# Kernel optimization log

Measured on AMD Instinct MI355X. Metric: run time of the kernel, lower is better.

The kernel has to match this reference:

```python
import jax, jax.numpy as jnp
import numpy as np

BN_EPS = 1e-5


def _gcn_layer(x, adj_norm, W, b, gamma, beta):
    # x: [B,T,V,C], adj_norm: [B,V,V] (identical per time step, as in the torch expand)
    x = jnp.einsum('bvw,btwc->btvc', adj_norm, x)
    x = jnp.einsum('btvc,co->btvo', x, W) + b
    # BatchNorm1d in training mode: biased batch stats over (B, T*V) per channel
    mean = x.mean(axis=(0, 1, 2))
    var = x.var(axis=(0, 1, 2))
    x = (x - mean) * jax.lax.rsqrt(var + BN_EPS) * gamma + beta
    return jax.nn.relu(x)


def _forward(x, adjacency, w1, b1, g1, be1, w2, b2, g2, be2, tw, tb, f1w, f1b, f2w, f2b):
    # degree-normalized adjacency: D^-1/2 A D^-1/2 (computed once; the torch
    # code recomputes the identical result inside B*T python loops)
    deg = adjacency.sum(axis=-1, keepdims=True)                # [B,V,1]
    dis = jnp.power(deg + 1e-6, -0.5)
    adj_norm = dis * adjacency * jnp.swapaxes(dis, -1, -2)     # [B,V,V]
    x1 = _gcn_layer(x, adj_norm, w1, b1, g1, be1)
    x2 = _gcn_layer(x1, adj_norm, w2, b2, g2, be2)
    x = x1 + x2                                                # [B,T,V,H]
    B, T, V, C = x.shape
    x = x.transpose(0, 2, 3, 1).reshape(B, V * C, T)           # [B, V*H, T]
    x = jax.lax.conv_general_dilated(
        x, tw, window_strides=(1,), padding=[(1, 1)],
        dimension_numbers=('NCH', 'OIH', 'NCH')) + tb[None, :, None]
    x = x.mean(axis=-1)                                        # [B, tcn_hidden]
    # dropout is identity in eval mode
    x = jax.nn.relu(x @ f1w + f1b)
    return x @ f2w + f2b


def setup_inputs() -> dict:
    key = jax.random.key(0)
    ks = jax.random.split(key, 12)
    B, T, V, Cin, H, TC, NC, K = 16, 512, 64, 16, 64, 256, 10, 3
    s = 0.05
    return {
        'x': jax.random.normal(ks[0], (B, T, V, Cin), jnp.float32),
        'adjacency': jax.random.uniform(ks[1], (B, V, V), jnp.float32),
        'w1': jax.random.normal(ks[2], (Cin, H), jnp.float32) * s,
        'b1': jnp.zeros((H,), jnp.float32),
        'g1': jnp.ones((H,), jnp.float32),
        'be1': jnp.zeros((H,), jnp.float32),
        'w2': jax.random.normal(ks[3], (H, H), jnp.float32) * s,
        'b2': jnp.zeros((H,), jnp.float32),
        'g2': jnp.ones((H,), jnp.float32),
        'be2': jnp.zeros((H,), jnp.float32),
        'tw': jax.random.normal(ks[4], (TC, H * V, K), jnp.float32) * 0.01,
        'tb': jnp.zeros((TC,), jnp.float32),
        'f1w': jax.random.normal(ks[5], (TC, TC // 2), jnp.float32) * s,
        'f1b': jnp.zeros((TC // 2,), jnp.float32),
        'f2w': jax.random.normal(ks[6], (TC // 2, NC), jnp.float32) * s,
        'f2b': jnp.zeros((NC,), jnp.float32),
    }


def reference(x, adjacency, w1, b1, g1, be1, w2, b2, g2, be2, tw, tb, f1w, f1b, f2w, f2b):
    return _forward(x, adjacency, w1, b1, g1, be1, w2, b2, g2, be2, tw, tb, f1w, f1b, f2w, f2b)
```

## Files before the change

kernel.cpp:

```cpp
#include <hip/hip_runtime.h>

#define B_   16
#define T_   512
#define V_   64
#define C1_  16
#define H_   64
#define TC_  256
#define NC_  10
#define INV_N (1.0f/524288.0f)
#define INV_T (1.0f/512.0f)

__global__ __launch_bounds__(256) void k_adjnorm(const float* __restrict__ adj,
                                                 float* __restrict__ AnT,
                                                 float* __restrict__ statsP) {
  const int b = blockIdx.x;
  __shared__ float As[4096];
  __shared__ float dis[64];
  for (int idx = threadIdx.x; idx < 4096; idx += 256) As[idx] = adj[b * 4096 + idx];
  __syncthreads();
  if (threadIdx.x < 64) {
    const int v = threadIdx.x;
    float s = 0.f;
    #pragma unroll 8
    for (int w = 0; w < 64; ++w) s += As[v * 64 + ((w + v) & 63)];
    dis[v] = rsqrtf(s + 1e-6f);
  }
  __syncthreads();
  for (int idx = threadIdx.x; idx < 4096; idx += 256) {
    const int v = idx >> 6, w = idx & 63;
    AnT[b * 4096 + w * 64 + v] = dis[v] * As[v * 64 + w] * dis[w];
  }
  if (threadIdx.x < 128) statsP[b * 128 + threadIdx.x] = 0.f;
}

__global__ __launch_bounds__(256) void k_gcn1(const float* __restrict__ x,
    const float* __restrict__ AnT, float* __restrict__ y) {
  const int b    = blockIdx.y;
  const int lane = threadIdx.x & 63;
  const int wq   = __builtin_amdgcn_readfirstlane(threadIdx.x >> 6);
  const float* __restrict__ At = AnT + b * 4096;
  for (int k = 0; k < 2; ++k) {
    const int t = blockIdx.x * 8 + wq * 2 + k;
    const float* __restrict__ xt = x + ((size_t)(b * T_ + t)) * V_ * C1_;
    float Y[16];
    #pragma unroll
    for (int i = 0; i < 16; ++i) Y[i] = 0.f;
    for (int w = 0; w < V_; ++w) {
      const float a = At[w * 64 + lane];
      const float* __restrict__ xr = xt + w * C1_;
      #pragma unroll
      for (int c = 0; c < 16; ++c) Y[c] += a * xr[c];
    }
    float4* yo = (float4*)(y + (((size_t)(b * T_ + t)) * V_ + lane) * C1_);
    yo[0] = make_float4(Y[0], Y[1], Y[2], Y[3]);
    yo[1] = make_float4(Y[4], Y[5], Y[6], Y[7]);
    yo[2] = make_float4(Y[8], Y[9], Y[10], Y[11]);
    yo[3] = make_float4(Y[12], Y[13], Y[14], Y[15]);
  }
}

__global__ __launch_bounds__(256) void k_stats1(const float* __restrict__ y,
    const float* __restrict__ w1, const float* __restrict__ b1,
    float* __restrict__ statsP) {
  const int lane = threadIdx.x & 63;
  const int wq   = __builtin_amdgcn_readfirstlane(threadIdx.x >> 6);
  float w1col[16];
  #pragma unroll
  for (int c = 0; c < 16; ++c) w1col[c] = w1[c * 64 + lane];
  const float bb = b1[lane];
  float ts0 = 0.f, ts1 = 0.f;
  const int row0 = blockIdx.x * 512 + wq * 128;
  for (int r = 0; r < 128; ++r) {
    const float* __restrict__ yr = y + (size_t)(row0 + r) * C1_;
    float z = bb;
    #pragma unroll
    for (int c = 0; c < 16; ++c) z += yr[c] * w1col[c];
    ts0 += z; ts1 += z * z;
  }
  __shared__ float sred[4][128];
  sred[wq][lane]      = ts0;
  sred[wq][64 + lane] = ts1;
  __syncthreads();
  if (threadIdx.x < 128) {
    const float v = sred[0][threadIdx.x] + sred[1][threadIdx.x] +
                    sred[2][threadIdx.x] + sred[3][threadIdx.x];
    atomicAdd(&statsP[(blockIdx.x & 7) * 128 + threadIdx.x], v);
  }
}

__global__ __launch_bounds__(256, 3) void k_gcn2(const float* __restrict__ y,
    const float* __restrict__ AnT, const float* __restrict__ w1,
    const float* __restrict__ b1, const float* __restrict__ g1,
    const float* __restrict__ be1, const float* __restrict__ w2,
    const float* __restrict__ b2, float* __restrict__ statsP,
    float* __restrict__ z2) {
  __shared__ float x1s[4096];
  __shared__ float Pt[64][65];
  __shared__ float aff[128];
  const int b    = blockIdx.y;
  const int t0   = blockIdx.x * 4;
  const int lane = threadIdx.x & 63;
  const int wq   = __builtin_amdgcn_readfirstlane(threadIdx.x >> 6);
  const int q0   = wq * 16;
  if (threadIdx.x < 64) {
    const int c = threadIdx.x;
    float s0 = 0.f, s1 = 0.f;
    #pragma unroll
    for (int s = 0; s < 8; ++s) { s0 += statsP[s * 128 + c]; s1 += statsP[s * 128 + 64 + c]; }
    const float mean = s0 * INV_N;
    const float var  = s1 * INV_N - mean * mean;
    const float sc   = g1[c] * rsqrtf(var + 1e-5f);
    aff[c]      = sc;
    aff[64 + c] = be1[c] - mean * sc + sc * b1[c];
  }
  __syncthreads();
  const float sc1 = aff[lane];
  const float shb = aff[64 + lane];
  float w1col[16];
  #pragma unroll
  for (int c = 0; c < 16; ++c) w1col[c] = w1[c * 64 + lane];
  const float* __restrict__ At = AnT + b * 4096;
  float ts0[16], ts1[16];
  #pragma unroll
  for (int i = 0; i < 16; ++i) { ts0[i] = 0.f; ts1[i] = 0.f; }

  for (int tt = 0; tt < 4; ++tt) {
    const int t = t0 + tt;
    const float* __restrict__ yt = y + ((size_t)(b * T_ + t)) * V_ * C1_;
    #pragma unroll
    for (int k = 0; k < 16; ++k) {
      const int w = q0 + k;
      const float* __restrict__ yr = yt + w * C1_;
      float z = 0.f;
      #pragma unroll
      for (int c = 0; c < 16; ++c) z += yr[c] * w1col[c];
      x1s[w * 64 + lane] = fmaxf(z * sc1 + shb, 0.f);
    }
    __syncthreads();
    float P[16];
    #pragma unroll
    for (int i = 0; i < 16; ++i) P[i] = 0.f;
    for (int w = 0; w < 64; ++w) {
      const float xv = x1s[w * 64 + lane];
      const float* __restrict__ ar = At + w * 64 + q0;
      #pragma unroll
      for (int i = 0; i < 16; ++i) P[i] += ar[i] * xv;
    }
    #pragma unroll
    for (int i = 0; i < 16; ++i) Pt[lane][q0 + i] = P[i];
    __syncthreads();
    float Z[16];
    #pragma unroll
    for (int i = 0; i < 16; ++i) Z[i] = b2[q0 + i];
    for (int c = 0; c < 64; ++c) {
      const float p = Pt[c][lane];
      const float* __restrict__ wr = w2 + c * 64 + q0;
      #pragma unroll
      for (int i = 0; i < 16; ++i) Z[i] += p * wr[i];
    }
    #pragma unroll
    for (int i = 0; i < 16; ++i) { const float v = Z[i]; ts0[i] += v; ts1[i] += v * v; }
    float4* zo = (float4*)(z2 + (((size_t)(b * T_ + t)) * V_ + lane) * H_ + q0);
    zo[0] = make_float4(Z[0], Z[1], Z[2], Z[3]);
    zo[1] = make_float4(Z[4], Z[5], Z[6], Z[7]);
    zo[2] = make_float4(Z[8], Z[9], Z[10], Z[11]);
    zo[3] = make_float4(Z[12], Z[13], Z[14], Z[15]);
    __syncthreads();
  }
  #pragma unroll
  for (int i = 0; i < 16; ++i) {
    float s0 = ts0[i], s1 = ts1[i];
    for (int off = 32; off > 0; off >>= 1) {
      s0 += __shfl_down(s0, off, 64);
      s1 += __shfl_down(s1, off, 64);
    }
    if (lane == 0) {
      atomicAdd(&statsP[(8 + (blockIdx.x & 7)) * 128 + q0 + i], s0);
      atomicAdd(&statsP[(8 + (blockIdx.x & 7)) * 128 + 64 + q0 + i], s1);
    }
  }
}

__global__ __launch_bounds__(256) void k_sfl(const float* __restrict__ y,
    const float* __restrict__ z2, const float* __restrict__ statsP,
    const float* __restrict__ w1, const float* __restrict__ b1,
    const float* __restrict__ g1, const float* __restrict__ be1,
    const float* __restrict__ g2, const float* __restrict__ be2,
    float* __restrict__ S, float* __restrict__ F, float* __restrict__ L) {
  const int b = blockIdx.y, v = blockIdx.x;
  const int c  = threadIdx.x & 63;
  const int wq = __builtin_amdgcn_readfirstlane(threadIdx.x >> 6);
  float s0 = 0.f, s1 = 0.f, u0 = 0.f, u1 = 0.f;
  #pragma unroll
  for (int s = 0; s < 8; ++s) {
    s0 += statsP[s * 128 + c];       s1 += statsP[s * 128 + 64 + c];
    u0 += statsP[(8 + s) * 128 + c]; u1 += statsP[(8 + s) * 128 + 64 + c];
  }
  const float m1 = s0 * INV_N, va1 = s1 * INV_N - m1 * m1;
  const float sc1  = g1[c] * rsqrtf(va1 + 1e-5f);
  const float shb1 = be1[c] - m1 * sc1 + sc1 * b1[c];
  const float m2 = u0 * INV_N, va2 = u1 * INV_N - m2 * m2;
  const float sc2 = g2[c] * rsqrtf(va2 + 1e-5f);
  const float sh2 = be2[c] - m2 * sc2;
  float w1col[16];
  #pragma unroll
  for (int cc = 0; cc < 16; ++cc) w1col[cc] = w1[cc * 64 + c];

  float acc = 0.f, fv = 0.f, lv = 0.f;
  for (int t = wq; t < T_; t += 4) {
    const size_t row = ((size_t)(b * T_ + t)) * V_ + v;
    const float* __restrict__ yr = y + row * C1_;
    float z1v = 0.f;
    #pragma unroll
    for (int cc = 0; cc < 16; ++cc) z1v += yr[cc] * w1col[cc];
    const float x1 = fmaxf(z1v * sc1 + shb1, 0.f);
    const float x2 = fmaxf(z2[row * H_ + c] * sc2 + sh2, 0.f);
    const float xs = x1 + x2;
    acc += xs;
    if (t == 0) fv = xs;
    if (t == T_ - 1) lv = xs;
  }
  __shared__ float red[4][64];
  red[wq][c] = acc;
  __syncthreads();
  const int o = (b * V_ + v) * 64 + c;
  if (wq == 0) { S[o] = red[0][c] + red[1][c] + red[2][c] + red[3][c]; F[o] = fv; }
  if (wq == 3) L[o] = lv;
}

__global__ __launch_bounds__(256) void k_pool(const float* __restrict__ S,
    const float* __restrict__ F, const float* __restrict__ L,
    const float* __restrict__ twt, float* __restrict__ mp) {
  const int cog = blockIdx.x;
  const int kc  = blockIdx.y;
  const int ci0 = kc * 256;
  __shared__ float a_s[3][16 * 260];
  for (int f4 = threadIdx.x; f4 < 3072; f4 += 256) {
    const int arr = f4 >> 10;
    const int rem = f4 & 1023;
    const int bb  = rem >> 6;
    const int ci4 = rem & 63;
    const float4 sv = *(const float4*)&S[bb * 4096 + ci0 + ci4 * 4];
    float4 o;
    if (arr == 0) {
      const float4 lv = *(const float4*)&L[bb * 4096 + ci0 + ci4 * 4];
      o = make_float4(sv.x - lv.x, sv.y - lv.y, sv.z - lv.z, sv.w - lv.w);
    } else if (arr == 1) {
      o = sv;
    } else {
      const float4 fvv = *(const float4*)&F[bb * 4096 + ci0 + ci4 * 4];
      o = make_float4(sv.x - fvv.x, sv.y - fvv.y, sv.z - fvv.z, sv.w - fvv.w);
    }
    *(float4*)&a_s[arr][bb * 260 + ci4 * 4] = o;
  }
  __syncthreads();
  const int bb   = threadIdx.x & 15;
  const int co   = threadIdx.x >> 4;
  const int co_g = cog * 16 + co;
  float acc = 0.f;
  for (int ci4 = 0; ci4 < 64; ++ci4) {
    const float4 a0 = *(const float4*)&a_s[0][bb * 260 + ci4 * 4];
    const float4 a1 = *(const float4*)&a_s[1][bb * 260 + ci4 * 4];
    const float4 a2 = *(const float4*)&a_s[2][bb * 260 + ci4 * 4];
    const float4* tp = (const float4*)(twt + ((size_t)co_g * 4096 + ci0 + ci4 * 4) * 3);
    const float4 f0 = tp[0], f1 = tp[1], f2 = tp[2];
    acc += f0.x * a0.x + f0.y * a1.x + f0.z * a2.x
         + f0.w * a0.y + f1.x * a1.y + f1.y * a2.y
         + f1.z * a0.z + f1.w * a1.z + f2.x * a2.z
         + f2.y * a0.w + f2.z * a1.w + f2.w * a2.w;
  }
  mp[kc * 4096 + bb * 256 + co_g] = acc;
}

__global__ __launch_bounds__(128) void k_head(const float* __restrict__ mp,
    const float* __restrict__ tb, const float* __restrict__ f1w,
    const float* __restrict__ f1b, const float* __restrict__ f2w,
    const float* __restrict__ f2b, float* __restrict__ out) {
  const int b = blockIdx.x;
  __shared__ float ms[256];
  __shared__ float hs[128];
  for (int co = threadIdx.x; co < 256; co += 128) {
    float s = 0.f;
    #pragma unroll
    for (int kc = 0; kc < 16; ++kc) s += mp[kc * 4096 + b * 256 + co];
    ms[co] = s * INV_T + tb[co];
  }
  __syncthreads();
  {
    const int j = threadIdx.x;
    float acc = f1b[j];
    #pragma unroll 8
    for (int k = 0; k < 256; ++k) acc += ms[k] * f1w[k * 128 + j];
    hs[j] = fmaxf(acc, 0.f);
  }
  __syncthreads();
  if (threadIdx.x < NC_) {
    const int n = threadIdx.x;
    float acc = f2b[n];
    #pragma unroll 8
    for (int j = 0; j < 128; ++j) acc += hs[j] * f2w[j * NC_ + n];
    out[b * NC_ + n] = acc;
  }
}

extern "C" void kernel_launch(void* const* d_in, const int* in_sizes, int n_in,
                              void* d_out, int out_size, void* d_ws, size_t ws_size,
                              hipStream_t stream) {
  const float* x   = (const float*)d_in[0];
  const float* adj = (const float*)d_in[1];
  const float* w1  = (const float*)d_in[2];
  const float* b1  = (const float*)d_in[3];
  const float* g1  = (const float*)d_in[4];
  const float* be1 = (const float*)d_in[5];
  const float* w2  = (const float*)d_in[6];
  const float* b2  = (const float*)d_in[7];
  const float* g2  = (const float*)d_in[8];
  const float* be2 = (const float*)d_in[9];
  const float* twt = (const float*)d_in[10];
  const float* tb  = (const float*)d_in[11];
  const float* f1w = (const float*)d_in[12];
  const float* f1b = (const float*)d_in[13];
  const float* f2w = (const float*)d_in[14];
  const float* f2b = (const float*)d_in[15];
  float* out = (float*)d_out;
  float* ws  = (float*)d_ws;

  float* AnT    = ws;
  float* statsP = ws + 65536;
  float* S      = ws + 67584;
  float* F      = ws + 133120;
  float* L      = ws + 198656;
  float* mp     = ws + 264192;
  float* y      = ws + 329728;
  float* z2     = y + (size_t)B_ * T_ * V_ * C1_;

  hipLaunchKernelGGL(k_adjnorm, dim3(B_), dim3(256), 0, stream, adj, AnT, statsP);
  hipLaunchKernelGGL(k_gcn1, dim3(T_ / 8, B_), dim3(256), 0, stream, x, AnT, y);
  hipLaunchKernelGGL(k_stats1, dim3(1024), dim3(256), 0, stream, y, w1, b1, statsP);
  hipLaunchKernelGGL(k_gcn2, dim3(T_ / 4, B_), dim3(256), 0, stream,
                     y, AnT, w1, b1, g1, be1, w2, b2, statsP, z2);
  hipLaunchKernelGGL(k_sfl, dim3(V_, B_), dim3(256), 0, stream,
                     y, z2, statsP, w1, b1, g1, be1, g2, be2, S, F, L);
  hipLaunchKernelGGL(k_pool, dim3(16, 16), dim3(256), 0, stream, S, F, L, twt, mp);
  hipLaunchKernelGGL(k_head, dim3(B_), dim3(128), 0, stream, mp, tb, f1w, f1b, f2w, f2b, out);
}
```

Baseline: 528.9 us.

## Compute layer-1 BN stats from input Gram matrix and restructure gcn2 and sfl

Replaces the layer-1 statistics pass with a kernel that accumulates per-channel sums and a 16x16 Gram matrix of the aggregated input. The mean and variance of y@W1 are then derived algebraically, so the 64-wide projection is not recomputed just for statistics. k_gcn2 now processes 8 timesteps per block and stages y through padded shared memory. A tiny k_aff kernel precomputes both BN affine coefficients, and k_sfl assigns timesteps to lanes with 64 per-thread accumulators reduced by shuffles. The trade-off is heavy register pressure and many cross-lane shuffles in the Gram and sfl kernels, plus an extra launch.

```diff
diff --git a/kernel.cpp b/kernel.cpp
--- a/kernel.cpp
+++ b/kernel.cpp
@@ -10,6 +10,7 @@
 #define INV_N (1.0f/524288.0f)
 #define INV_T (1.0f/512.0f)
 
+
 __global__ __launch_bounds__(256) void k_adjnorm(const float* __restrict__ adj,
                                                  float* __restrict__ AnT,
                                                  float* __restrict__ statsP) {
@@ -30,7 +31,7 @@
     const int v = idx >> 6, w = idx & 63;
     AnT[b * 4096 + w * 64 + v] = dis[v] * As[v * 64 + w] * dis[w];
   }
-  if (threadIdx.x < 128) statsP[b * 128 + threadIdx.x] = 0.f;
+  if (threadIdx.x < 140) statsP[b * 140 + threadIdx.x] = 0.f;
 }
 
 __global__ __launch_bounds__(256) void k_gcn1(const float* __restrict__ x,
@@ -59,104 +60,147 @@
   }
 }
 
-__global__ __launch_bounds__(256) void k_stats1(const float* __restrict__ y,
-    const float* __restrict__ w1, const float* __restrict__ b1,
-    float* __restrict__ statsP) {
-  const int lane = threadIdx.x & 63;
-  const int wq   = __builtin_amdgcn_readfirstlane(threadIdx.x >> 6);
-  float w1col[16];
-  #pragma unroll
-  for (int c = 0; c < 16; ++c) w1col[c] = w1[c * 64 + lane];
-  const float bb = b1[lane];
-  float ts0 = 0.f, ts1 = 0.f;
-  const int row0 = blockIdx.x * 512 + wq * 128;
-  for (int r = 0; r < 128; ++r) {
-    const float* __restrict__ yr = y + (size_t)(row0 + r) * C1_;
-    float z = bb;
-    #pragma unroll
-    for (int c = 0; c < 16; ++c) z += yr[c] * w1col[c];
-    ts0 += z; ts1 += z * z;
-  }
-  __shared__ float sred[4][128];
-  sred[wq][lane]      = ts0;
-  sred[wq][64 + lane] = ts1;
-  __syncthreads();
-  if (threadIdx.x < 128) {
-    const float v = sred[0][threadIdx.x] + sred[1][threadIdx.x] +
-                    sred[2][threadIdx.x] + sred[3][threadIdx.x];
-    atomicAdd(&statsP[(blockIdx.x & 7) * 128 + threadIdx.x], v);
-  }
-}
-
-__global__ __launch_bounds__(256, 3) void k_gcn2(const float* __restrict__ y,
+__global__ __launch_bounds__(256) void k_gram(const float* __restrict__ y,
+                                              float* __restrict__ statsP) {
+  const int tid = blockIdx.x * 256 + threadIdx.x;
+  const float* __restrict__ yp = y + (size_t)tid * 64;
+  float sy[16], G[136];
+  #pragma unroll
+  for (int i = 0; i < 16; ++i) sy[i] = 0.f;
+  #pragma unroll
+  for (int i = 0; i < 136; ++i) G[i] = 0.f;
+  #pragma unroll
+  for (int r = 0; r < 4; ++r) {
+    float v[16];
+    const float4* vp = (const float4*)(yp + r * 16);
+    const float4 a0 = vp[0], a1 = vp[1], a2 = vp[2], a3 = vp[3];
+    v[0]=a0.x; v[1]=a0.y; v[2]=a0.z; v[3]=a0.w;
+    v[4]=a1.x; v[5]=a1.y; v[6]=a1.z; v[7]=a1.w;
+    v[8]=a2.x; v[9]=a2.y; v[10]=a2.z; v[11]=a2.w;
+    v[12]=a3.x; v[13]=a3.y; v[14]=a3.z; v[15]=a3.w;
+    #pragma unroll
+    for (int c = 0; c < 16; ++c) sy[c] += v[c];
+    int idx = 0;
+    #pragma unroll
+    for (int c = 0; c < 16; ++c)
+      #pragma unroll
+      for (int d = c; d < 16; ++d) { G[idx] += v[c] * v[d]; ++idx; }
+  }
+  #pragma unroll
+  for (int m = 1; m <= 32; m <<= 1) {
+    #pragma unroll
+    for (int i = 0; i < 16; ++i) sy[i] += __shfl_xor(sy[i], m, 64);
+    #pragma unroll
+    for (int i = 0; i < 136; ++i) G[i] += __shfl_xor(G[i], m, 64);
+  }
+  if ((threadIdx.x & 63) == 0) {
+    float* sp = statsP + (blockIdx.x & 7) * 152;
+    #pragma unroll
+    for (int i = 0; i < 16; ++i) atomicAdd(&sp[i], sy[i]);
+    #pragma unroll
+    for (int i = 0; i < 136; ++i) atomicAdd(&sp[16 + i], G[i]);
+  }
+}
+
+__global__ __launch_bounds__(256) void k_gcn2(const float* __restrict__ y,
     const float* __restrict__ AnT, const float* __restrict__ w1,
     const float* __restrict__ b1, const float* __restrict__ g1,
     const float* __restrict__ be1, const float* __restrict__ w2,
     const float* __restrict__ b2, float* __restrict__ statsP,
     float* __restrict__ z2) {
-  __shared__ float x1s[4096];
-  __shared__ float Pt[64][65];
-  __shared__ float aff[128];
+  __shared__ float ybuf[64 * 17];
+  __shared__ float sbuf[64 * 65];
+  __shared__ float gtot[152];
+  __shared__ float affl[128];
   const int b    = blockIdx.y;
-  const int t0   = blockIdx.x * 4;
+  const int t0   = blockIdx.x * 8;
   const int lane = threadIdx.x & 63;
   const int wq   = __builtin_amdgcn_readfirstlane(threadIdx.x >> 6);
   const int q0   = wq * 16;
+
+  for (int i = threadIdx.x; i < 152; i += 256) {
+    float s = 0.f;
+    #pragma unroll
+    for (int sl = 0; sl < 8; ++sl) s += statsP[sl * 152 + i];
+    gtot[i] = s;
+  }
+  __syncthreads();
   if (threadIdx.x < 64) {
-    const int c = threadIdx.x;
-    float s0 = 0.f, s1 = 0.f;
-    #pragma unroll
-    for (int s = 0; s < 8; ++s) { s0 += statsP[s * 128 + c]; s1 += statsP[s * 128 + 64 + c]; }
-    const float mean = s0 * INV_N;
-    const float var  = s1 * INV_N - mean * mean;
-    const float sc   = g1[c] * rsqrtf(var + 1e-5f);
-    aff[c]      = sc;
-    aff[64 + c] = be1[c] - mean * sc + sc * b1[c];
-  }
-  __syncthreads();
-  const float sc1 = aff[lane];
-  const float shb = aff[64 + lane];
-  float w1col[16];
-  #pragma unroll
-  for (int c = 0; c < 16; ++c) w1col[c] = w1[c * 64 + lane];
+    const int o = threadIdx.x;
+    float wv[16];
+    #pragma unroll
+    for (int c = 0; c < 16; ++c) wv[c] = w1[c * 64 + o];
+    float lin = 0.f;
+    #pragma unroll
+    for (int c = 0; c < 16; ++c) lin += gtot[c] * wv[c];
+    float qd = 0.f;
+    int idx = 16;
+    #pragma unroll
+    for (int c = 0; c < 16; ++c) {
+      qd += gtot[idx] * wv[c] * wv[c]; ++idx;
+      #pragma unroll
+      for (int d = c + 1; d < 16; ++d) { qd += 2.f * gtot[idx] * wv[c] * wv[d]; ++idx; }
+    }
+    const float linN = lin * INV_N;
+    const float mean = linN + b1[o];
+    const float var  = qd * INV_N - linN * linN;
+    const float sc   = g1[o] * rsqrtf(var + 1e-5f);
+    const float sh   = be1[o] - mean * sc;
+    affl[o] = sc; affl[64 + o] = sh;
+    statsP[2240 + o] = sc; statsP[2304 + o] = sh;
+  }
+  __syncthreads();
+  float asc[16], ash[16];
+  #pragma unroll
+  for (int i = 0; i < 16; ++i) { asc[i] = affl[q0 + i]; ash[i] = affl[64 + q0 + i]; }
+
   const float* __restrict__ At = AnT + b * 4096;
   float ts0[16], ts1[16];
   #pragma unroll
   for (int i = 0; i < 16; ++i) { ts0[i] = 0.f; ts1[i] = 0.f; }
 
-  for (int tt = 0; tt < 4; ++tt) {
+  for (int tt = 0; tt < 8; ++tt) {
     const int t = t0 + tt;
-    const float* __restrict__ yt = y + ((size_t)(b * T_ + t)) * V_ * C1_;
+    const float4 yv4 = *(const float4*)(y + ((size_t)(b * T_ + t)) * 1024 + threadIdx.x * 4);
+    __syncthreads();
+    { const int w = threadIdx.x >> 2, c0 = (threadIdx.x & 3) * 4;
+      ybuf[w * 17 + c0 + 0] = yv4.x;
+      ybuf[w * 17 + c0 + 1] = yv4.y;
+      ybuf[w * 17 + c0 + 2] = yv4.z;
+      ybuf[w * 17 + c0 + 3] = yv4.w; }
+    __syncthreads();
+    float z[16];
+    #pragma unroll
+    for (int i = 0; i < 16; ++i) z[i] = 0.f;
     #pragma unroll
     for (int k = 0; k < 16; ++k) {
-      const int w = q0 + k;
-      const float* __restrict__ yr = yt + w * C1_;
-      float z = 0.f;
-      #pragma unroll
-      for (int c = 0; c < 16; ++c) z += yr[c] * w1col[c];
-      x1s[w * 64 + lane] = fmaxf(z * sc1 + shb, 0.f);
-    }
+      const float yk = ybuf[lane * 17 + k];
+      #pragma unroll
+      for (int i = 0; i < 16; ++i) z[i] += yk * w1[k * 64 + q0 + i];
+    }
+    #pragma unroll
+    for (int i = 0; i < 16; ++i)
+      sbuf[lane * 65 + q0 + i] = fmaxf(z[i] * asc[i] + ash[i], 0.f);
     __syncthreads();
     float P[16];
     #pragma unroll
     for (int i = 0; i < 16; ++i) P[i] = 0.f;
     for (int w = 0; w < 64; ++w) {
-      const float xv = x1s[w * 64 + lane];
-      const float* __restrict__ ar = At + w * 64 + q0;
-      #pragma unroll
-      for (int i = 0; i < 16; ++i) P[i] += ar[i] * xv;
-    }
-    #pragma unroll
-    for (int i = 0; i < 16; ++i) Pt[lane][q0 + i] = P[i];
+      const float xv = sbuf[w * 65 + lane];
+      #pragma unroll
+      for (int i = 0; i < 16; ++i) P[i] += At[w * 64 + q0 + i] * xv;
+    }
+    __syncthreads();
+    #pragma unroll
+    for (int i = 0; i < 16; ++i) sbuf[(q0 + i) * 65 + lane] = P[i];
     __syncthreads();
     float Z[16];
     #pragma unroll
     for (int i = 0; i < 16; ++i) Z[i] = b2[q0 + i];
     for (int c = 0; c < 64; ++c) {
-      const float p = Pt[c][lane];
-      const float* __restrict__ wr = w2 + c * 64 + q0;
-      #pragma unroll
-      for (int i = 0; i < 16; ++i) Z[i] += p * wr[i];
+      const float p = sbuf[lane * 65 + c];
+      #pragma unroll
+      for (int i = 0; i < 16; ++i) Z[i] += w2[c * 64 + q0 + i] * p;
     }
     #pragma unroll
     for (int i = 0; i < 16; ++i) { const float v = Z[i]; ts0[i] += v; ts1[i] += v * v; }
@@ -165,7 +209,6 @@
     zo[1] = make_float4(Z[4], Z[5], Z[6], Z[7]);
     zo[2] = make_float4(Z[8], Z[9], Z[10], Z[11]);
     zo[3] = make_float4(Z[12], Z[13], Z[14], Z[15]);
-    __syncthreads();
   }
   #pragma unroll
   for (int i = 0; i < 16; ++i) {
@@ -175,57 +218,86 @@
       s1 += __shfl_down(s1, off, 64);
     }
     if (lane == 0) {
-      atomicAdd(&statsP[(8 + (blockIdx.x & 7)) * 128 + q0 + i], s0);
-      atomicAdd(&statsP[(8 + (blockIdx.x & 7)) * 128 + 64 + q0 + i], s1);
-    }
+      atomicAdd(&statsP[1216 + (blockIdx.x & 7) * 128 + q0 + i], s0);
+      atomicAdd(&statsP[1216 + (blockIdx.x & 7) * 128 + 64 + q0 + i], s1);
+    }
+  }
+}
+
+__global__ void k_aff(const float* __restrict__ g2, const float* __restrict__ be2,
+                      float* __restrict__ statsP) {
+  const int o = threadIdx.x;
+  if (o < 64) {
+    float u0 = 0.f, u1 = 0.f;
+    #pragma unroll
+    for (int sl = 0; sl < 8; ++sl) {
+      u0 += statsP[1216 + sl * 128 + o];
+      u1 += statsP[1216 + sl * 128 + 64 + o];
+    }
+    const float m2 = u0 * INV_N;
+    const float va = u1 * INV_N - m2 * m2;
+    const float sc = g2[o] * rsqrtf(va + 1e-5f);
+    statsP[2368 + o] = sc;
+    statsP[2432 + o] = be2[o] - m2 * sc;
   }
 }
 
 __global__ __launch_bounds__(256) void k_sfl(const float* __restrict__ y,
     const float* __restrict__ z2, const float* __restrict__ statsP,
-    const float* __restrict__ w1, const float* __restrict__ b1,
-    const float* __restrict__ g1, const float* __restrict__ be1,
-    const float* __restrict__ g2, const float* __restrict__ be2,
+    const float* __restrict__ w1,
     float* __restrict__ S, float* __restrict__ F, float* __restrict__ L) {
   const int b = blockIdx.y, v = blockIdx.x;
-  const int c  = threadIdx.x & 63;
-  const int wq = __builtin_amdgcn_readfirstlane(threadIdx.x >> 6);
-  float s0 = 0.f, s1 = 0.f, u0 = 0.f, u1 = 0.f;
-  #pragma unroll
-  for (int s = 0; s < 8; ++s) {
-    s0 += statsP[s * 128 + c];       s1 += statsP[s * 128 + 64 + c];
-    u0 += statsP[(8 + s) * 128 + c]; u1 += statsP[(8 + s) * 128 + 64 + c];
-  }
-  const float m1 = s0 * INV_N, va1 = s1 * INV_N - m1 * m1;
-  const float sc1  = g1[c] * rsqrtf(va1 + 1e-5f);
-  const float shb1 = be1[c] - m1 * sc1 + sc1 * b1[c];
-  const float m2 = u0 * INV_N, va2 = u1 * INV_N - m2 * m2;
-  const float sc2 = g2[c] * rsqrtf(va2 + 1e-5f);
-  const float sh2 = be2[c] - m2 * sc2;
-  float w1col[16];
-  #pragma unroll
-  for (int cc = 0; cc < 16; ++cc) w1col[cc] = w1[cc * 64 + c];
-
-  float acc = 0.f, fv = 0.f, lv = 0.f;
-  for (int t = wq; t < T_; t += 4) {
+  const int lane = threadIdx.x & 63;
+  const int wq   = __builtin_amdgcn_readfirstlane(threadIdx.x >> 6);
+  float acc[64];
+  #pragma unroll
+  for (int i = 0; i < 64; ++i) acc[i] = 0.f;
+  __shared__ float red[4][64];
+  #pragma unroll
+  for (int j = 0; j < 2; ++j) {
+    const int t = wq * 128 + lane * 2 + j;
     const size_t row = ((size_t)(b * T_ + t)) * V_ + v;
-    const float* __restrict__ yr = y + row * C1_;
-    float z1v = 0.f;
-    #pragma unroll
-    for (int cc = 0; cc < 16; ++cc) z1v += yr[cc] * w1col[cc];
-    const float x1 = fmaxf(z1v * sc1 + shb1, 0.f);
-    const float x2 = fmaxf(z2[row * H_ + c] * sc2 + sh2, 0.f);
-    const float xs = x1 + x2;
-    acc += xs;
-    if (t == 0) fv = xs;
-    if (t == T_ - 1) lv = xs;
-  }
-  __shared__ float red[4][64];
-  red[wq][c] = acc;
-  __syncthreads();
-  const int o = (b * V_ + v) * 64 + c;
-  if (wq == 0) { S[o] = red[0][c] + red[1][c] + red[2][c] + red[3][c]; F[o] = fv; }
-  if (wq == 3) L[o] = lv;
+    float yv[16];
+    { const float4* yp = (const float4*)(y + row * 16);
+      const float4 a0 = yp[0], a1 = yp[1], a2 = yp[2], a3 = yp[3];
+      yv[0]=a0.x; yv[1]=a0.y; yv[2]=a0.z; yv[3]=a0.w;
+      yv[4]=a1.x; yv[5]=a1.y; yv[6]=a1.z; yv[7]=a1.w;
+      yv[8]=a2.x; yv[9]=a2.y; yv[10]=a2.z; yv[11]=a2.w;
+      yv[12]=a3.x; yv[13]=a3.y; yv[14]=a3.z; yv[15]=a3.w; }
+    #pragma unroll
+    for (int cq = 0; cq < 16; ++cq) {
+      const float4 z2v = *(const float4*)(z2 + row * 64 + cq * 4);
+      #pragma unroll
+      for (int jj = 0; jj < 4; ++jj) {
+        const int ch = cq * 4 + jj;
+        float z1 = 0.f;
+        #pragma unroll
+        for (int k = 0; k < 16; ++k) z1 += yv[k] * w1[k * 64 + ch];
+        const float x1 = fmaxf(z1 * statsP[2240 + ch] + statsP[2304 + ch], 0.f);
+        const float zz = (jj == 0) ? z2v.x : (jj == 1) ? z2v.y : (jj == 2) ? z2v.z : z2v.w;
+        const float x2 = fmaxf(zz * statsP[2368 + ch] + statsP[2432 + ch], 0.f);
+        const float xs = x1 + x2;
+        acc[ch] += xs;
+        if (t == 0)        F[(b * V_ + v) * 64 + ch] = xs;
+        if (t == T_ - 1)   L[(b * V_ + v) * 64 + ch] = xs;
+      }
+    }
+  }
+  #pragma unroll
+  for (int ch = 0; ch < 64; ++ch) {
+    float s = acc[ch];
+    #pragma unroll
+    for (int m = 1; m <= 32; m <<= 1) s += __shfl_xor(s, m, 64);
+    acc[ch] = s;
+  }
+  if (lane == 0) {
+    #pragma unroll
+    for (int ch = 0; ch < 64; ++ch) red[wq][ch] = acc[ch];
+  }
+  __syncthreads();
+  if (threadIdx.x < 64)
+    S[(b * V_ + v) * 64 + threadIdx.x] = red[0][threadIdx.x] + red[1][threadIdx.x] +
+                                         red[2][threadIdx.x] + red[3][threadIdx.x];
 }
 
 __global__ __launch_bounds__(256) void k_pool(const float* __restrict__ S,
@@ -327,20 +399,21 @@
 
   float* AnT    = ws;
   float* statsP = ws + 65536;
-  float* S      = ws + 67584;
-  float* F      = ws + 133120;
-  float* L      = ws + 198656;
-  float* mp     = ws + 264192;
-  float* y      = ws + 329728;
+  float* S      = ws + 68096;
+  float* F      = ws + 133632;
+  float* L      = ws + 199168;
+  float* mp     = ws + 264704;
+  float* y      = ws + 330240;
   float* z2     = y + (size_t)B_ * T_ * V_ * C1_;
 
   hipLaunchKernelGGL(k_adjnorm, dim3(B_), dim3(256), 0, stream, adj, AnT, statsP);
   hipLaunchKernelGGL(k_gcn1, dim3(T_ / 8, B_), dim3(256), 0, stream, x, AnT, y);
-  hipLaunchKernelGGL(k_stats1, dim3(1024), dim3(256), 0, stream, y, w1, b1, statsP);
-  hipLaunchKernelGGL(k_gcn2, dim3(T_ / 4, B_), dim3(256), 0, stream,
+  hipLaunchKernelGGL(k_gram, dim3(512), dim3(256), 0, stream, y, statsP);
+  hipLaunchKernelGGL(k_gcn2, dim3(T_ / 8, B_), dim3(256), 0, stream,
                      y, AnT, w1, b1, g1, be1, w2, b2, statsP, z2);
+  hipLaunchKernelGGL(k_aff, dim3(1), dim3(64), 0, stream, g2, be2, statsP);
   hipLaunchKernelGGL(k_sfl, dim3(V_, B_), dim3(256), 0, stream,
-                     y, z2, statsP, w1, b1, g1, be1, g2, be2, S, F, L);
+                     y, z2, statsP, w1, S, F, L);
   hipLaunchKernelGGL(k_pool, dim3(16, 16), dim3(256), 0, stream, S, F, L, twt, mp);
   hipLaunchKernelGGL(k_head, dim3(B_), dim3(128), 0, stream, mp, tb, f1w, f1b, f2w, f2b, out);
 }
```

After: 826.2 us. 1.56x slower.
